# Kernel tuning notes

Measured on AMD Instinct MI355X. Metric: run time of the kernel, lower is better.

## Reference

```python
import jax, jax.numpy as jnp
import numpy as np

B, S, D = 8, 1024, 1024
H, DK = 16, 64  # num_heads, d_k; H*DK == D
NEG_INF = 1e29


def setup_inputs() -> dict:
    key = jax.random.key(0)
    ks = jax.random.split(key, 12)
    sc = 1.0 / np.sqrt(D)
    q = jax.random.normal(ks[0], (B, S, D), jnp.float32)
    k = jax.random.normal(ks[1], (B, S, D), jnp.float32)
    v = jax.random.normal(ks[2], (B, S, D), jnp.float32)
    # causal mask, broadcast per batch (mask==0 positions are masked out)
    mask = jnp.broadcast_to(jnp.tril(jnp.ones((S, S), jnp.int32)), (B, S, S))
    Wq = jax.random.normal(ks[3], (D, D), jnp.float32) * sc
    bq = jax.random.normal(ks[4], (D,), jnp.float32) * 0.01
    Wk = jax.random.normal(ks[5], (D, D), jnp.float32) * sc
    bk = jax.random.normal(ks[6], (D,), jnp.float32) * 0.01
    Wv = jax.random.normal(ks[7], (D, D), jnp.float32) * sc
    bv = jax.random.normal(ks[8], (D,), jnp.float32) * 0.01
    Wo = jax.random.normal(ks[9], (D, D), jnp.float32) * sc
    bo = jax.random.normal(ks[10], (D,), jnp.float32) * 0.01
    return {"q": q, "k": k, "v": v, "mask": mask,
            "Wq": Wq, "bq": bq, "Wk": Wk, "bk": bk,
            "Wv": Wv, "bv": bv, "Wo": Wo, "bo": bo}


def reference(q, k, v, mask, Wq, bq, Wk, bk, Wv, bv, Wo, bo):
    # Linear projections (torch Linear: x @ W.T + b)
    q1 = q @ Wq.T + bq
    k1 = k @ Wk.T + bk
    v1 = v @ Wv.T + bv
    # [B, S, D] -> [B, H, S, DK]
    def split_heads(x):
        return x.reshape(B, S, H, DK).transpose(0, 2, 1, 3)
    q3, k3, v3 = split_heads(q1), split_heads(k1), split_heads(v1)
    # scores [B, H, S, S]
    scores = jnp.einsum('bhqd,bhkd->bhqk', q3, k3) / jnp.sqrt(jnp.float32(DK))
    scores = jnp.where(mask[:, None, :, :] == 0, -NEG_INF, scores)
    probs = jax.nn.softmax(scores, axis=-1)
    attn = jnp.einsum('bhqk,bhkd->bhqd', probs, v3)  # [B, H, S, DK]
    out = attn.transpose(0, 2, 1, 3).reshape(B, S, D)
    return out @ Wo.T + bo
```

## Files before the change

kernel.cpp:

```cpp
#include <hip/hip_runtime.h>
#include <hip/hip_bf16.h>
#include <stdint.h>

constexpr int NB = 8;
constexpr int NS = 1024;
constexpr int ND = 1024;
constexpr int NH = 16;
constexpr int NDK = 64;
constexpr int NT = NS / 64;
constexpr int NKT = ND / 64;

typedef __bf16 bf16_t;
typedef __attribute__((ext_vector_type(8))) __bf16 bf16x8;
typedef __attribute__((ext_vector_type(4))) __bf16 bf16x4;
typedef __attribute__((ext_vector_type(4))) float f32x4;

#define GLL16(g, s) __builtin_amdgcn_global_load_lds( \
    (const __attribute__((address_space(1))) void*)(g), \
    (__attribute__((address_space(3))) void*)(s), 16, 0, 0)

__device__ __forceinline__ void cvt_body(const float* __restrict__ s,
                                         bf16_t* __restrict__ d, long n) {
  long i0 = (long)(blockIdx.x * blockDim.x + threadIdx.x) * 4;
  long step = (long)gridDim.x * blockDim.x * 4;
  for (long i = i0; i < n; i += step) {
    float4 f = *(const float4*)(s + i);
    bf16x4 o;
    o[0] = (bf16_t)f.x; o[1] = (bf16_t)f.y; o[2] = (bf16_t)f.z; o[3] = (bf16_t)f.w;
    *(bf16x4*)(d + i) = o;
  }
}

__global__ __launch_bounds__(256) void cvt4_kernel(const float* s0, bf16_t* d0,
                                                   const float* s1, bf16_t* d1,
                                                   const float* s2, bf16_t* d2,
                                                   const float* s3, bf16_t* d3, long n) {
  const float* s = blockIdx.y == 0 ? s0 : blockIdx.y == 1 ? s1 : blockIdx.y == 2 ? s2 : s3;
  bf16_t* d = blockIdx.y == 0 ? d0 : blockIdx.y == 1 ? d1 : blockIdx.y == 2 ? d2 : d3;
  cvt_body(s, d, n);
}

__global__ __launch_bounds__(512, 2) void gemm_qkv(
    const float* A0, const bf16_t* W0, const float* b0, bf16_t* C0,
    const float* A1, const bf16_t* W1, const float* b1, bf16_t* C1,
    const float* A2, const bf16_t* W2, const float* b2, bf16_t* C2) {
  __shared__ bf16_t S[2 * 16384 + 3 * 8192];
  const int o = blockIdx.x;
  const int xcd = o & 7, s = o >> 3;
  const int bx = s & 7, u = s >> 3;
  const int zby = xcd + 8 * u;
  const int z = zby >> 5, by = zby & 31;
  const float* A = z == 0 ? A0 : z == 1 ? A1 : A2;
  const bf16_t* W = z == 0 ? W0 : z == 1 ? W1 : W2;
  const float* bb = z == 0 ? b0 : z == 1 ? b1 : b2;
  bf16_t* C = z == 0 ? C0 : z == 1 ? C1 : C2;

  const int tid = threadIdx.x;
  const int l = tid & 63, w = tid >> 6;
  const int wr = w >> 1, wc = w & 1;
  const int g = l >> 4, r = l & 15;
  const int m0 = by * 256, n0 = bx * 128;
  const int wbase = w * 512;

  bf16_t* Ab = S;
  bf16_t* Bb = S + 32768;

  float4 faA[8], faB[8];
  auto issueA = [&](int t, float4 (&dst)[8]) {
#pragma unroll
    for (int it = 0; it < 4; ++it) {
      const float* p = A + (size_t)(m0 + it * 64 + (tid >> 3)) * ND + t * 64 + (tid & 7) * 8;
      dst[it * 2]     = *(const float4*)p;
      dst[it * 2 + 1] = *(const float4*)(p + 4);
    }
  };
  auto writeA = [&](int ab, float4 (&src)[8]) {
#pragma unroll
    for (int it = 0; it < 4; ++it) {
      int row = it * 64 + (tid >> 3), c = tid & 7;
      bf16x8 ov;
      ov[0] = (bf16_t)src[it * 2].x;     ov[1] = (bf16_t)src[it * 2].y;
      ov[2] = (bf16_t)src[it * 2].z;     ov[3] = (bf16_t)src[it * 2].w;
      ov[4] = (bf16_t)src[it * 2 + 1].x; ov[5] = (bf16_t)src[it * 2 + 1].y;
      ov[6] = (bf16_t)src[it * 2 + 1].z; ov[7] = (bf16_t)src[it * 2 + 1].w;
      *(bf16x8*)(Ab + ab * 16384 + row * 64 + ((c ^ (row & 7)) << 3)) = ov;
    }
  };
  auto stageB = [&](int qb, int t) {
#pragma unroll
    for (int it = 0; it < 2; ++it) {
      int idx = it * 512 + tid;
      int row = idx >> 3, c = (idx & 7) ^ (row & 7);
      GLL16(W + (size_t)(n0 + row) * ND + (t << 6) + c * 8,
            Bb + qb * 8192 + it * 4096 + wbase);
    }
  };

  f32x4 acc[4][4] = {};

  issueA(0, faA);
  issueA(1, faB);
  stageB(0, 0);
  stageB(1, 1);
  asm volatile("s_waitcnt vmcnt(2)" ::: "memory");
  __builtin_amdgcn_sched_barrier(0);
  writeA(0, faA);
  asm volatile("s_waitcnt lgkmcnt(0)" ::: "memory");
  __builtin_amdgcn_s_barrier();

  auto bodyT = [&](int t, float4 (&fiss)[8], float4 (&fwr)[8]) {
    if (t + 2 < NKT) issueA(t + 2, fiss);
    __builtin_amdgcn_sched_barrier(0);
    if (t + 2 < NKT) stageB((t + 2) % 3, t + 2);
    __builtin_amdgcn_sched_barrier(0);

    const bf16_t* a_ = Ab + (t & 1) * 16384;
    const bf16_t* b_ = Bb + (t % 3) * 8192;
#pragma unroll
    for (int kk = 0; kk < 2; ++kk) {
      bf16x8 af[4], bw[4];
#pragma unroll
      for (int m = 0; m < 4; ++m) {
        int row = wr * 64 + m * 16 + r;
        af[m] = *(const bf16x8*)(a_ + row * 64 + (((kk * 4 + g) ^ (row & 7)) << 3));
      }
#pragma unroll
      for (int n = 0; n < 4; ++n) {
        int row = wc * 64 + n * 16 + r;
        bw[n] = *(const bf16x8*)(b_ + row * 64 + (((kk * 4 + g) ^ (row & 7)) << 3));
      }
      __builtin_amdgcn_s_setprio(1);
#pragma unroll
      for (int m = 0; m < 4; ++m)
#pragma unroll
        for (int n = 0; n < 4; ++n)
          acc[m][n] = __builtin_amdgcn_mfma_f32_16x16x32_bf16(af[m], bw[n], acc[m][n], 0, 0, 0);
      __builtin_amdgcn_s_setprio(0);
    }

    if (t + 2 < NKT)      asm volatile("s_waitcnt vmcnt(10)" ::: "memory");
    else                  asm volatile("s_waitcnt vmcnt(0)" ::: "memory");
    __builtin_amdgcn_sched_barrier(0);
    if (t + 1 < NKT) writeA((t + 1) & 1, fwr);
    asm volatile("s_waitcnt lgkmcnt(0)" ::: "memory");
    __builtin_amdgcn_s_barrier();
  };

#pragma unroll 1
  for (int tt = 0; tt < NKT; tt += 2) {
    bodyT(tt, faA, faB);
    bodyT(tt + 1, faB, faA);
  }

#pragma unroll
  for (int n = 0; n < 4; ++n) {
    int col = n0 + wc * 64 + n * 16 + r;
    float bv = bb[col];
#pragma unroll
    for (int m = 0; m < 4; ++m) {
      int row0 = m0 + wr * 64 + m * 16 + g * 4;
#pragma unroll
      for (int j = 0; j < 4; ++j)
        C[(size_t)(row0 + j) * ND + col] = (bf16_t)(acc[m][n][j] + bv);
    }
  }
}

__global__ __launch_bounds__(512, 2) void gemm_bt(const bf16_t* __restrict__ A,
                                                  const bf16_t* __restrict__ W,
                                                  const float* __restrict__ bias,
                                                  float* __restrict__ Cout,
                                                  int M, int N, int K) {
  __shared__ bf16_t S[3 * 24576];
  const int o = blockIdx.x;
  const int xcd = o & 7, s = o >> 3;
  const int bx = s & 7, u = s >> 3;
  const int by = xcd + 8 * u;

  const int tid = threadIdx.x;
  const int l = tid & 63, w = tid >> 6;
  const int wr = w >> 1, wc = w & 1;
  const int g = l >> 4, r = l & 15;
  const int m0 = by * 256, n0 = bx * 128;
  const int wbase = w * 512;

  auto stageA2 = [&](int q, int t, int half) {
#pragma unroll
    for (int it = half * 2; it < half * 2 + 2; ++it) {
      int idx = it * 512 + tid;
      int row = idx >> 3, c = (idx & 7) ^ (row & 7);
      GLL16(A + (size_t)(m0 + row) * K + (t << 6) + c * 8,
            S + q * 24576 + it * 4096 + wbase);
    }
  };
  auto stageB2 = [&](int q, int t) {
#pragma unroll
    for (int it = 0; it < 2; ++it) {
      int idx = it * 512 + tid;
      int row = idx >> 3, c = (idx & 7) ^ (row & 7);
      GLL16(W + (size_t)(n0 + row) * K + (t << 6) + c * 8,
            S + q * 24576 + 16384 + it * 4096 + wbase);
    }
  };

  f32x4 acc[4][4] = {};
  const int NKT2 = K >> 6;

  stageA2(0, 0, 0); stageA2(0, 0, 1); stageB2(0, 0);
  stageA2(1, 1, 0); stageA2(1, 1, 1); stageB2(1, 1);

  int q = 0;
  for (int t = 0; t < NKT2; ++t) {
    const bool pf = (t + 2 < NKT2);
    int q2 = q + 2; if (q2 >= 3) q2 -= 3;

    if (t + 1 < NKT2) asm volatile("s_waitcnt vmcnt(6)" ::: "memory");
    else              asm volatile("s_waitcnt vmcnt(0)" ::: "memory");
    __builtin_amdgcn_s_barrier();

    const bf16_t* a_ = S + q * 24576;
    const bf16_t* b_ = a_ + 16384;

#pragma unroll
    for (int kk = 0; kk < 2; ++kk) {
      bf16x8 bw[4];
#pragma unroll
      for (int n = 0; n < 4; ++n) {
        int row = wc * 64 + n * 16 + r;
        bw[n] = *(const bf16x8*)(b_ + row * 64 + (((kk * 4 + g) ^ (row & 7)) << 3));
      }
#pragma unroll
      for (int mh = 0; mh < 2; ++mh) {
        bf16x8 af[2];
#pragma unroll
        for (int i = 0; i < 2; ++i) {
          int row = wr * 64 + (mh * 2 + i) * 16 + r;
          af[i] = *(const bf16x8*)(a_ + row * 64 + (((kk * 4 + g) ^ (row & 7)) << 3));
        }
        if (pf) {
          int ph = kk * 2 + mh;
          if (ph == 0)      stageA2(q2, t + 2, 0);
          else if (ph == 1) stageA2(q2, t + 2, 1);
          else if (ph == 2) stageB2(q2, t + 2);
        }
        __builtin_amdgcn_s_barrier();
        asm volatile("s_waitcnt lgkmcnt(0)" ::: "memory");
        __builtin_amdgcn_sched_barrier(0);
        __builtin_amdgcn_s_setprio(1);
#pragma unroll
        for (int i = 0; i < 2; ++i)
#pragma unroll
          for (int n = 0; n < 4; ++n)
            acc[mh * 2 + i][n] = __builtin_amdgcn_mfma_f32_16x16x32_bf16(
                af[i], bw[n], acc[mh * 2 + i][n], 0, 0, 0);
        __builtin_amdgcn_s_setprio(0);
        __builtin_amdgcn_sched_barrier(0);
      }
    }
    ++q; if (q >= 3) q -= 3;
  }

#pragma unroll
  for (int n = 0; n < 4; ++n) {
    int col = n0 + wc * 64 + n * 16 + r;
    float bv = bias[col];
#pragma unroll
    for (int m = 0; m < 4; ++m) {
      int row0 = m0 + wr * 64 + m * 16 + g * 4;
#pragma unroll
      for (int j = 0; j < 4; ++j)
        Cout[(size_t)(row0 + j) * N + col] = acc[m][n][j] + bv;
    }
  }
}

__global__ __launch_bounds__(256, 4) void attn_kernel(const bf16_t* __restrict__ Q1,
                                                      const bf16_t* __restrict__ K1,
                                                      const bf16_t* __restrict__ V1,
                                                      bf16_t* __restrict__ attn) {
  __shared__ bf16_t Kt[2][64 * 64];
  __shared__ bf16_t Vt[2][64 * 64];
  __shared__ bf16_t Pl[4][16 * 64];

  const int tid = threadIdx.x;
  const int l = tid & 63, w = tid >> 6;
  const int g = l >> 4, r = l & 15;

  const int o = blockIdx.x;
  const int os = (o & 7) * 128 + (o >> 3);
  const int pair = os & 7, hb = os >> 3;
  const int h = hb & 15, b = hb >> 4;

  constexpr float SC = 0.18033688011112042f;

  for (int ph = 0; ph < 2; ++ph) {
    const int qt = ph ? (NT - 1 - pair) : pair;
    const int qrow_g = qt * 64 + w * 16 + r;

    const bf16_t* qptr = Q1 + ((size_t)b * NS + qrow_g) * ND + h * 64;
    bf16x8 qf0 = *(const bf16x8*)(qptr + g * 8);
    bf16x8 qf1 = *(const bf16x8*)(qptr + 32 + g * 8);
#pragma unroll
    for (int i = 0; i < 8; ++i) {
      qf0[i] = (bf16_t)((float)qf0[i] * SC);
      qf1[i] = (bf16_t)((float)qf1[i] * SC);
    }

    float mrun = -1e30f, lrun = 0.f;
    f32x4 oacc[4] = {};

    __syncthreads();

    bf16x8 vr0, vr1;
    {
#pragma unroll
      for (int it = 0; it < 2; ++it) {
        int idx = it * 256 + tid;
        int key = idx >> 3;
        int dkg = ((idx & 7) ^ (key & 7)) << 3;
        GLL16(K1 + ((size_t)b * NS + key) * ND + h * 64 + dkg,
              &Kt[0][(it * 256 + w * 64) * 8]);
      }
      vr0 = *(const bf16x8*)(V1 + ((size_t)b * NS + l) * ND + h * 64 + w * 8);
      vr1 = *(const bf16x8*)(V1 + ((size_t)b * NS + l) * ND + h * 64 + (4 + w) * 8);
    }

    for (int kt = 0; kt <= qt; ++kt) {
      const int p = kt & 1;
      const int k0 = kt * 64;

#pragma unroll
      for (int it = 0; it < 2; ++it) {
        int dkb = (it * 4 + w) * 8;
#pragma unroll
        for (int jj = 0; jj < 8; ++jj) {
          int dk = dkb + jj;
          int boff = dk * 128 + ((l * 2) ^ ((dk & 7) << 4));
          *(bf16_t*)((char*)Vt[p] + boff) = (it ? vr1 : vr0)[jj];
        }
      }
      __syncthreads();

      if (kt < qt) {
        const int k0n = k0 + 64;
#pragma unroll
        for (int it = 0; it < 2; ++it) {
          int idx = it * 256 + tid;
          int key = idx >> 3;
          int dkg = ((idx & 7) ^ (key & 7)) << 3;
          GLL16(K1 + ((size_t)b * NS + k0n + key) * ND + h * 64 + dkg,
                &Kt[p ^ 1][(it * 256 + w * 64) * 8]);
        }
        vr0 = *(const bf16x8*)(V1 + ((size_t)b * NS + k0n + l) * ND + h * 64 + w * 8);
        vr1 = *(const bf16x8*)(V1 + ((size_t)b * NS + k0n + l) * ND + h * 64 + (4 + w) * 8);
      }

      f32x4 sacc[4] = {};
      __builtin_amdgcn_s_setprio(1);
#pragma unroll
      for (int n = 0; n < 4; ++n) {
        int key = n * 16 + r;
#pragma unroll
        for (int kk = 0; kk < 2; ++kk) {
          int dk2 = kk * 32 + g * 8;
          int boff = key * 128 + ((dk2 * 2) ^ ((key & 7) << 4));
          bf16x8 kf = *(const bf16x8*)((char*)Kt[p] + boff);
          sacc[n] = __builtin_amdgcn_mfma_f32_16x16x32_bf16(kf, kk == 0 ? qf0 : qf1, sacc[n], 0, 0, 0);
        }
      }
      __builtin_amdgcn_s_setprio(0);

      if (kt == qt) {
#pragma unroll
        for (int n = 0; n < 4; ++n)
#pragma unroll
          for (int j = 0; j < 4; ++j)
            if (k0 + n * 16 + g * 4 + j > qrow_g) sacc[n][j] = -1e30f;
      }

      float mx;
      {
        float t0 = fmaxf(fmaxf(sacc[0][0], sacc[0][1]), fmaxf(sacc[0][2], sacc[0][3]));
        float t1 = fmaxf(fmaxf(sacc[1][0], sacc[1][1]), fmaxf(sacc[1][2], sacc[1][3]));
        float t2 = fmaxf(fmaxf(sacc[2][0], sacc[2][1]), fmaxf(sacc[2][2], sacc[2][3]));
        float t3 = fmaxf(fmaxf(sacc[3][0], sacc[3][1]), fmaxf(sacc[3][2], sacc[3][3]));
        mx = fmaxf(fmaxf(t0, t1), fmaxf(t2, t3));
      }
      mx = fmaxf(mx, __shfl_xor(mx, 16));
      mx = fmaxf(mx, __shfl_xor(mx, 32));

      if (!__all(mx <= mrun + 8.0f)) {
        float m_new = fmaxf(mrun, mx);
        float esc = __builtin_amdgcn_exp2f(mrun - m_new);
        mrun = m_new;
        lrun *= esc;
#pragma unroll
        for (int n = 0; n < 4; ++n)
#pragma unroll
          for (int j = 0; j < 4; ++j) oacc[n][j] *= esc;
      }

      float rsum = 0.f;
#pragma unroll
      for (int n = 0; n < 4; ++n) {
        bf16x4 p4;
#pragma unroll
        for (int j = 0; j < 4; ++j) {
          float pe = __builtin_amdgcn_exp2f(sacc[n][j] - mrun);
          rsum += pe;
          p4[j] = (bf16_t)pe;
        }
        *(bf16x4*)((char*)Pl[w] + r * 128 + ((n * 32 + g * 8) ^ ((r & 7) << 4))) = p4;
      }
      rsum += __shfl_xor(rsum, 16);
      rsum += __shfl_xor(rsum, 32);
      lrun += rsum;

      __builtin_amdgcn_s_setprio(1);
#pragma unroll
      for (int kk = 0; kk < 2; ++kk) {
        bf16x8 pf = *(const bf16x8*)((char*)Pl[w] + r * 128 + ((kk * 64 + g * 16) ^ ((r & 7) << 4)));
#pragma unroll
        for (int n = 0; n < 4; ++n) {
          int dkr = n * 16 + r;
          bf16x8 vf = *(const bf16x8*)((char*)Vt[p] + dkr * 128 + ((kk * 64 + g * 16) ^ ((r & 7) << 4)));
          oacc[n] = __builtin_amdgcn_mfma_f32_16x16x32_bf16(vf, pf, oacc[n], 0, 0, 0);
        }
      }
      __builtin_amdgcn_s_setprio(0);
    }

    float linv = 1.0f / lrun;
#pragma unroll
    for (int n = 0; n < 4; ++n) {
      bf16x4 o4;
#pragma unroll
      for (int j = 0; j < 4; ++j) o4[j] = (bf16_t)(oacc[n][j] * linv);
      *(bf16x4*)(attn + ((size_t)b * NS + qrow_g) * ND + h * 64 + n * 16 + g * 4) = o4;
    }
  }
}

extern "C" void kernel_launch(void* const* d_in, const int* in_sizes, int n_in,
                              void* d_out, int out_size, void* d_ws, size_t ws_size,
                              hipStream_t stream) {
  const float* q  = (const float*)d_in[0];
  const float* k  = (const float*)d_in[1];
  const float* v  = (const float*)d_in[2];
  const float* Wq = (const float*)d_in[4];
  const float* bq = (const float*)d_in[5];
  const float* Wk = (const float*)d_in[6];
  const float* bk = (const float*)d_in[7];
  const float* Wv = (const float*)d_in[8];
  const float* bv = (const float*)d_in[9];
  const float* Wo = (const float*)d_in[10];
  const float* bo = (const float*)d_in[11];
  float* out = (float*)d_out;

  const size_t NX = (size_t)NB * NS * ND;
  const size_t NW = (size_t)ND * ND;
  char* ws = (char*)d_ws;
  size_t off = 0;
  auto alloc = [&](size_t bytes) {
    char* p = ws + off;
    off += (bytes + 255) & ~(size_t)255;
    return p;
  };
  bf16_t* wqb = (bf16_t*)alloc(NW * 2);
  bf16_t* wkb = (bf16_t*)alloc(NW * 2);
  bf16_t* wvb = (bf16_t*)alloc(NW * 2);
  bf16_t* wob = (bf16_t*)alloc(NW * 2);
  bf16_t* q1  = (bf16_t*)alloc(NX * 2);
  bf16_t* k1  = (bf16_t*)alloc(NX * 2);
  bf16_t* v1  = (bf16_t*)alloc(NX * 2);
  bf16_t* at  = (bf16_t*)alloc(NX * 2);

  dim3 blk(256);
  cvt4_kernel<<<dim3(128, 4), blk, 0, stream>>>(Wq, wqb, Wk, wkb, Wv, wvb, Wo, wob, (long)NW);

  gemm_qkv<<<dim3(768), dim3(512), 0, stream>>>(
      q, wqb, bq, q1, k, wkb, bk, k1, v, wvb, bv, v1);

  attn_kernel<<<dim3((NT / 2) * NH * NB), blk, 0, stream>>>(q1, k1, v1, at);

  gemm_bt<<<dim3(256), dim3(512), 0, stream>>>(at, wob, bo, out, NB * NS, ND, ND);
}
```

Baseline: 149.4 us.

## Write V projection transposed per head and async-load it in attention

The QKV GEMM epilogue now writes the V projection in a [B,H,DK,S] transposed layout. The attention kernel can then stage V tiles into LDS with the same swizzled global_load_lds path used for K, instead of loading V into registers and scattering it with per-element LDS writes. This removes the register round trip and the scalar LDS stores from the attention inner loop, and lets V loads overlap compute asynchronously. The cost is that the V GEMM epilogue does strided 8-byte stores along the sequence dimension, which may coalesce less well.

```diff
diff --git a/kernel.cpp b/kernel.cpp
--- a/kernel.cpp
+++ b/kernel.cpp
@@ -152,16 +152,34 @@
     bodyT(tt + 1, faB, faA);
   }
 
-#pragma unroll
-  for (int n = 0; n < 4; ++n) {
-    int col = n0 + wc * 64 + n * 16 + r;
-    float bv = bb[col];
-#pragma unroll
-    for (int m = 0; m < 4; ++m) {
-      int row0 = m0 + wr * 64 + m * 16 + g * 4;
-#pragma unroll
-      for (int j = 0; j < 4; ++j)
-        C[(size_t)(row0 + j) * ND + col] = (bf16_t)(acc[m][n][j] + bv);
+  if (z == 2) {
+#pragma unroll
+    for (int n = 0; n < 4; ++n) {
+      int col = n0 + wc * 64 + n * 16 + r;
+      int hh = col >> 6, dk = col & 63;
+      float bv = bb[col];
+#pragma unroll
+      for (int m = 0; m < 4; ++m) {
+        int row0 = m0 + wr * 64 + m * 16 + g * 4;
+        int b_ = row0 >> 10, s0 = row0 & 1023;
+        bf16x4 o4;
+#pragma unroll
+        for (int j = 0; j < 4; ++j) o4[j] = (bf16_t)(acc[m][n][j] + bv);
+        *(bf16x4*)(C + (((size_t)b_ * 16 + hh) * 64 + dk) * 1024 + s0) = o4;
+      }
+    }
+  } else {
+#pragma unroll
+    for (int n = 0; n < 4; ++n) {
+      int col = n0 + wc * 64 + n * 16 + r;
+      float bv = bb[col];
+#pragma unroll
+      for (int m = 0; m < 4; ++m) {
+        int row0 = m0 + wr * 64 + m * 16 + g * 4;
+#pragma unroll
+        for (int j = 0; j < 4; ++j)
+          C[(size_t)(row0 + j) * ND + col] = (bf16_t)(acc[m][n][j] + bv);
+      }
     }
   }
 }
@@ -276,7 +294,7 @@
 
 __global__ __launch_bounds__(256, 4) void attn_kernel(const bf16_t* __restrict__ Q1,
                                                       const bf16_t* __restrict__ K1,
-                                                      const bf16_t* __restrict__ V1,
+                                                      const bf16_t* __restrict__ V1t,
                                                       bf16_t* __restrict__ attn) {
   __shared__ bf16_t Kt[2][64 * 64];
   __shared__ bf16_t Vt[2][64 * 64];
@@ -292,6 +310,7 @@
   const int h = hb & 15, b = hb >> 4;
 
   constexpr float SC = 0.18033688011112042f;
+  const bf16_t* vbase = V1t + ((size_t)(b * 16 + h) * 64) * 1024;
 
   for (int ph = 0; ph < 2; ++ph) {
     const int qt = ph ? (NT - 1 - pair) : pair;
@@ -311,49 +330,35 @@
 
     __syncthreads();
 
-    bf16x8 vr0, vr1;
-    {
+    auto stageKV = [&](int kt2, int pb) {
+      const int k0 = kt2 * 64;
 #pragma unroll
       for (int it = 0; it < 2; ++it) {
         int idx = it * 256 + tid;
-        int key = idx >> 3;
-        int dkg = ((idx & 7) ^ (key & 7)) << 3;
-        GLL16(K1 + ((size_t)b * NS + key) * ND + h * 64 + dkg,
-              &Kt[0][(it * 256 + w * 64) * 8]);
-      }
-      vr0 = *(const bf16x8*)(V1 + ((size_t)b * NS + l) * ND + h * 64 + w * 8);
-      vr1 = *(const bf16x8*)(V1 + ((size_t)b * NS + l) * ND + h * 64 + (4 + w) * 8);
-    }
+        int row = idx >> 3;
+        int c = (idx & 7) ^ (row & 7);
+        GLL16(K1 + ((size_t)b * NS + k0 + row) * ND + h * 64 + c * 8,
+              &Kt[pb][(it * 256 + w * 64) * 8]);
+      }
+#pragma unroll
+      for (int it = 0; it < 2; ++it) {
+        int idx = it * 256 + tid;
+        int row = idx >> 3;
+        int c = (idx & 7) ^ (row & 7);
+        GLL16(vbase + (size_t)row * 1024 + k0 + c * 8,
+              &Vt[pb][(it * 256 + w * 64) * 8]);
+      }
+    };
+
+    stageKV(0, 0);
 
     for (int kt = 0; kt <= qt; ++kt) {
       const int p = kt & 1;
       const int k0 = kt * 64;
 
-#pragma unroll
-      for (int it = 0; it < 2; ++it) {
-        int dkb = (it * 4 + w) * 8;
-#pragma unroll
-        for (int jj = 0; jj < 8; ++jj) {
-          int dk = dkb + jj;
-          int boff = dk * 128 + ((l * 2) ^ ((dk & 7) << 4));
-          *(bf16_t*)((char*)Vt[p] + boff) = (it ? vr1 : vr0)[jj];
-        }
-      }
       __syncthreads();
 
-      if (kt < qt) {
-        const int k0n = k0 + 64;
-#pragma unroll
-        for (int it = 0; it < 2; ++it) {
-          int idx = it * 256 + tid;
-          int key = idx >> 3;
-          int dkg = ((idx & 7) ^ (key & 7)) << 3;
-          GLL16(K1 + ((size_t)b * NS + k0n + key) * ND + h * 64 + dkg,
-                &Kt[p ^ 1][(it * 256 + w * 64) * 8]);
-        }
-        vr0 = *(const bf16x8*)(V1 + ((size_t)b * NS + k0n + l) * ND + h * 64 + w * 8);
-        vr1 = *(const bf16x8*)(V1 + ((size_t)b * NS + k0n + l) * ND + h * 64 + (4 + w) * 8);
-      }
+      if (kt < qt) stageKV(kt + 1, p ^ 1);
 
       f32x4 sacc[4] = {};
       __builtin_amdgcn_s_setprio(1);
@@ -423,7 +428,7 @@
 #pragma unroll
         for (int n = 0; n < 4; ++n) {
           int dkr = n * 16 + r;
-          bf16x8 vf = *(const bf16x8*)((char*)Vt[p] + dkr * 128 + ((kk * 64 + g * 16) ^ ((r & 7) << 4)));
+          bf16x8 vf = *(const bf16x8*)((char*)Vt[p] + dkr * 128 + ((kk * 64 + g * 16) ^ ((dkr & 7) << 4)));
           oacc[n] = __builtin_amdgcn_mfma_f32_16x16x32_bf16(vf, pf, oacc[n], 0, 0, 0);
         }
       }
@@ -472,16 +477,16 @@
   bf16_t* wob = (bf16_t*)alloc(NW * 2);
   bf16_t* q1  = (bf16_t*)alloc(NX * 2);
   bf16_t* k1  = (bf16_t*)alloc(NX * 2);
-  bf16_t* v1  = (bf16_t*)alloc(NX * 2);
+  bf16_t* v1t = (bf16_t*)alloc(NX * 2);
   bf16_t* at  = (bf16_t*)alloc(NX * 2);
 
   dim3 blk(256);
   cvt4_kernel<<<dim3(128, 4), blk, 0, stream>>>(Wq, wqb, Wk, wkb, Wv, wvb, Wo, wob, (long)NW);
 
   gemm_qkv<<<dim3(768), dim3(512), 0, stream>>>(
-      q, wqb, bq, q1, k, wkb, bk, k1, v, wvb, bv, v1);
-
-  attn_kernel<<<dim3((NT / 2) * NH * NB), blk, 0, stream>>>(q1, k1, v1, at);
+      q, wqb, bq, q1, k, wkb, bk, k1, v, wvb, bv, v1t);
+
+  attn_kernel<<<dim3((NT / 2) * NH * NB), blk, 0, stream>>>(q1, k1, v1t, at);
 
   gemm_bt<<<dim3(256), dim3(512), 0, stream>>>(at, wob, bo, out, NB * NS, ND, ND);
 }
```

New measurement: 145.3 us. -2.7%, faster.
